# Kernel optimization log

Measured on AMD Instinct MI355X. Metric: run time of the kernel, lower is better.

The kernel has to match this reference:

```python
import jax, jax.numpy as jnp
import numpy as np

B = 64          # batch
NV = 6890       # SMPL vertices
NF = 13776      # SMPL faces
NHD = 20000     # HD (uniformly resampled) vertices
NP = 24         # SMPL parts
COP_W = 10.0
COP_K = 100.0
EPS = 1e-6


def setup_inputs() -> dict:
    key = jax.random.key(0)
    k1, k2, k3, k4, k5 = jax.random.split(key, 5)
    vertices = jax.random.normal(k1, (B, NV, 3), jnp.float32)
    hd_operator = jax.random.uniform(k2, (NHD, NV), jnp.float32) / NV
    faces = jax.random.randint(k3, (NF, 3), 0, NV)          # triangle vertex ids
    vert_fid = jax.random.randint(k4, (NHD,), 0, NF)        # HD vert -> source face
    face_part = jax.random.randint(k5, (NF,), 0, NP)        # face -> body part
    return {"vertices": vertices, "hd_operator": hd_operator,
            "faces": faces, "vert_fid": vert_fid, "face_part": face_part}


def reference(vertices, hd_operator, faces, vert_fid, face_part):
    # --- per-part volume: signed tetrahedron volume per face, summed per part ---
    tri = vertices[:, faces]                      # [B, NF, 3, 3]
    v0, v1, v2 = tri[:, :, 0], tri[:, :, 1], tri[:, :, 2]
    vol_f = jnp.abs(jnp.einsum('bfi,bfi->bf', v0, jnp.cross(v1, v2))) / 6.0  # [B, NF]
    part_onehot = jax.nn.one_hot(face_part, NP, dtype=vol_f.dtype)           # [NF, NP]
    per_part_volume = jnp.einsum('bf,fp->bp', vol_f, part_onehot)            # [B, NP]

    vertices_hd = jnp.einsum('nm,bmd->bnd', hd_operator, vertices)           # [B, NHD, 3]

    # --- map each HD vertex to the volume of its part ---
    part_of_vert = face_part[vert_fid]                                       # [NHD]
    vol_vert = per_part_volume[:, part_of_vert][..., None]                   # [B, NHD, 1]

    # --- volume-weighted COM ---
    com = jnp.sum(vertices_hd * vol_vert, axis=1) / jnp.sum(vol_vert, axis=1)  # [B, 3]

    # --- pressure-weighted COP ---
    h = vertices_hd[:, :, 1]  # vertex height above ground plane (y)
    pw = jnp.where(h < 0.0, 1.0 - COP_K * h, jnp.exp(-COP_W * h))            # [B, NHD]
    cop = jnp.sum(vertices_hd * pw[..., None], axis=1) / (
        jnp.sum(pw, axis=1, keepdims=True) + EPS)                            # [B, 3]

    # --- stability loss: xz distance between COM and COP ---
    d = com - cop
    return jnp.sqrt(d[:, 0] ** 2 + d[:, 2] ** 2)                             # [B]
```

## Files before the change

kernel.cpp:

```cpp
#include <hip/hip_runtime.h>
#include <cstdint>

#define B_    64
#define NV_   6890
#define NF_   13776
#define NHD_  20000
#define NP_   24
#define NCH   216
#define KSPL  4
#define CPW   54

#define OFF_PPV   0u
#define OFF_RED   6144u
#define ZERO_BYTES 7680u
#define OFF_VC    7680u

typedef __attribute__((ext_vector_type(8))) __bf16 bf16x8;
typedef __attribute__((ext_vector_type(8))) unsigned short u16x8;
typedef __attribute__((ext_vector_type(4))) float f32x4;

__device__ __forceinline__ unsigned short f2bf(float f) {
    unsigned u = __float_as_uint(f);
    u = (u + 0x7fffu + ((u >> 16) & 1u)) >> 16;
    return (unsigned short)u;
}

__global__ __launch_bounds__(256) void k0v_pack(const float* __restrict__ verts,
                                                unsigned short* __restrict__ Vc) {
    int idx = blockIdx.x * 256 + threadIdx.x;
    int j    = idx & 7;
    int lane = (idx >> 3) & 63;
    int ct   = idx >> 9;
    int t    = ct % 12;
    int c    = ct / 12;
    int lm   = lane & 15;
    int kk   = (lane >> 4) * 8 + j;
    int bd   = t * 16 + lm;
    int d    = bd >> 6, b = bd & 63;
    int k    = c * 32 + kk;
    float v  = (k < NV_) ? verts[((size_t)b * NV_ + k) * 3 + d] : 0.f;
    Vc[idx] = f2bf(v);
}

__global__ __launch_bounds__(256) void k1_vol(const float* __restrict__ verts,
                                              const int* __restrict__ faces,
                                              const int* __restrict__ face_part,
                                              float* __restrict__ ppv) {
    __shared__ float bins[NP_];
    int b = blockIdx.y;
    int f = blockIdx.x * 256 + threadIdx.x;
    if (threadIdx.x < NP_) bins[threadIdx.x] = 0.f;
    __syncthreads();
    if (f < NF_) {
        int i0 = faces[3 * f], i1 = faces[3 * f + 1], i2 = faces[3 * f + 2];
        const float* vb = verts + (size_t)b * NV_ * 3;
        float ax = vb[3 * i0], ay = vb[3 * i0 + 1], az = vb[3 * i0 + 2];
        float bx = vb[3 * i1], by = vb[3 * i1 + 1], bz = vb[3 * i1 + 2];
        float cx = vb[3 * i2], cy = vb[3 * i2 + 1], cz = vb[3 * i2 + 2];
        float crx = by * cz - bz * cy;
        float cry = bz * cx - bx * cz;
        float crz = bx * cy - by * cx;
        float vol = fabsf(ax * crx + ay * cry + az * crz) * (1.0f / 6.0f);
        atomicAdd(&bins[face_part[f]], vol);
    }
    __syncthreads();
    if (threadIdx.x < NP_) atomicAdd(&ppv[b * NP_ + threadIdx.x], bins[threadIdx.x]);
}

__global__ __launch_bounds__(256, 3) void kf_fused(const float* __restrict__ Hm,
                                                   const unsigned short* __restrict__ Vc,
                                                   const int* __restrict__ vert_fid,
                                                   const int* __restrict__ face_part,
                                                   const float* __restrict__ ppv,
                                                   float* __restrict__ red) {
    __shared__ float accs[16 * 192];
    __shared__ float reds[B_ * 6];
    const int tid  = threadIdx.x;
    const int lane = tid & 63;
    const int s    = tid >> 6;
    const int lm   = lane & 15;
    const int kg   = lane >> 4;
    const int n0   = blockIdx.x * 16;
    const float* Arow = Hm + (size_t)(n0 + lm) * NV_;

    const int cs = s * CPW, ce = cs + CPW;

    f32x4 acc[12];
#pragma unroll
    for (int t = 0; t < 12; ++t) acc[t] = (f32x4){0.f, 0.f, 0.f, 0.f};

    float2 a0, a1, a2, a3, na0, na1, na2, na3;

    auto issueA = [&](int c, float2& b0, float2& b1, float2& b2, float2& b3) {
        int k0 = c * 32 + kg * 8;
        if (c == NCH - 1) {
            float tf[8];
#pragma unroll
            for (int j = 0; j < 8; ++j) {
                int k = k0 + j;
                tf[j] = (k < NV_) ? Arow[k] : 0.f;
            }
            b0 = make_float2(tf[0], tf[1]); b1 = make_float2(tf[2], tf[3]);
            b2 = make_float2(tf[4], tf[5]); b3 = make_float2(tf[6], tf[7]);
        } else {
            b0 = *reinterpret_cast<const float2*>(Arow + k0);
            b1 = *reinterpret_cast<const float2*>(Arow + k0 + 2);
            b2 = *reinterpret_cast<const float2*>(Arow + k0 + 4);
            b3 = *reinterpret_cast<const float2*>(Arow + k0 + 6);
        }
    };

    issueA(cs, a0, a1, a2, a3);
    for (int c = cs; c < ce; ++c) {
        const u16x8* Bp = reinterpret_cast<const u16x8*>(Vc) + (size_t)c * 12 * 64 + lane;
        u16x8 Bu[12];
#pragma unroll
        for (int t = 0; t < 12; ++t) Bu[t] = Bp[t * 64];
        if (c + 1 < ce) issueA(c + 1, na0, na1, na2, na3);
        u16x8 au;
        au[0] = f2bf(a0.x); au[1] = f2bf(a0.y); au[2] = f2bf(a1.x); au[3] = f2bf(a1.y);
        au[4] = f2bf(a2.x); au[5] = f2bf(a2.y); au[6] = f2bf(a3.x); au[7] = f2bf(a3.y);
        bf16x8 Af = __builtin_bit_cast(bf16x8, au);
#pragma unroll
        for (int t = 0; t < 12; ++t)
            acc[t] = __builtin_amdgcn_mfma_f32_16x16x32_bf16(
                Af, __builtin_bit_cast(bf16x8, Bu[t]), acc[t], 0, 0, 0);
        a0 = na0; a1 = na1; a2 = na2; a3 = na3;
    }

    for (int i = tid; i < 16 * 192; i += 256) accs[i] = 0.f;
    for (int i = tid; i < B_ * 6; i += 256) reds[i] = 0.f;
    __syncthreads();
#pragma unroll
    for (int t = 0; t < 12; ++t)
#pragma unroll
        for (int r = 0; r < 4; ++r)
            atomicAdd(&accs[(kg * 4 + r) * 192 + t * 16 + lm], acc[t][r]);
    __syncthreads();

    {
        int b  = tid & 63;
        int r0 = tid >> 6;
        float scx = 0.f, scz = 0.f, smx = 0.f, smz = 0.f, ssp = 0.f, ssw = 0.f;
#pragma unroll
        for (int q = 0; q < 4; ++q) {
            int row = q * 4 + r0;
            int n = n0 + row;
            float x = accs[row * 192 + b];
            float h = accs[row * 192 + 64 + b];
            float z = accs[row * 192 + 128 + b];
            float pwv = (h < 0.f) ? (1.f - 100.f * h) : expf(-10.f * h);
            int part = face_part[vert_fid[n]];
            float w = ppv[b * NP_ + part];
            scx += pwv * x; scz += pwv * z;
            smx += w * x;   smz += w * z;
            ssp += pwv;     ssw += w;
        }
        atomicAdd(&reds[b * 6 + 0], scx);
        atomicAdd(&reds[b * 6 + 1], scz);
        atomicAdd(&reds[b * 6 + 2], smx);
        atomicAdd(&reds[b * 6 + 3], smz);
        atomicAdd(&reds[b * 6 + 4], ssp);
        atomicAdd(&reds[b * 6 + 5], ssw);
    }
    __syncthreads();
    for (int i = tid; i < B_ * 6; i += 256) atomicAdd(&red[i], reds[i]);
}

__global__ __launch_bounds__(64) void k5_final(const float* __restrict__ red,
                                               float* __restrict__ out) {
    int b = threadIdx.x;
    if (b < B_) {
        float sp   = red[b * 6 + 4] + 1e-6f;
        float sw   = red[b * 6 + 5];
        float copx = red[b * 6 + 0] / sp;
        float copz = red[b * 6 + 1] / sp;
        float comx = red[b * 6 + 2] / sw;
        float comz = red[b * 6 + 3] / sw;
        float dx = comx - copx, dz = comz - copz;
        out[b] = sqrtf(dx * dx + dz * dz);
    }
}

extern "C" void kernel_launch(void* const* d_in, const int* in_sizes, int n_in,
                              void* d_out, int out_size, void* d_ws, size_t ws_size,
                              hipStream_t stream) {
    const float* verts     = (const float*)d_in[0];
    const float* Hm        = (const float*)d_in[1];
    const int*   faces     = (const int*)d_in[2];
    const int*   vert_fid  = (const int*)d_in[3];
    const int*   face_part = (const int*)d_in[4];
    char* ws = (char*)d_ws;
    float*          ppv = (float*)(ws + OFF_PPV);
    float*          red = (float*)(ws + OFF_RED);
    unsigned short* Vc  = (unsigned short*)(ws + OFF_VC);
    float* out = (float*)d_out;

    hipMemsetAsync(d_ws, 0, ZERO_BYTES, stream);
    hipLaunchKernelGGL(k0v_pack, dim3((NCH * 12 * 512) / 256), dim3(256), 0, stream, verts, Vc);
    hipLaunchKernelGGL(k1_vol, dim3(54, 64), dim3(256), 0, stream, verts, faces, face_part, ppv);
    hipLaunchKernelGGL(kf_fused, dim3(NHD_ / 16), dim3(256), 0, stream,
                       Hm, Vc, vert_fid, face_part, ppv, red);
    hipLaunchKernelGGL(k5_final, dim3(1), dim3(64), 0, stream, red, out);
}
```

Before: 312.6 us.

## Process 32 HD rows per block to reuse packed vertex tiles across two MFMA sets

```diff
diff --git a/kernel.cpp b/kernel.cpp
--- a/kernel.cpp
+++ b/kernel.cpp
@@ -67,101 +67,116 @@
     if (threadIdx.x < NP_) atomicAdd(&ppv[b * NP_ + threadIdx.x], bins[threadIdx.x]);
 }
 
-__global__ __launch_bounds__(256, 3) void kf_fused(const float* __restrict__ Hm,
-                                                   const unsigned short* __restrict__ Vc,
-                                                   const int* __restrict__ vert_fid,
-                                                   const int* __restrict__ face_part,
-                                                   const float* __restrict__ ppv,
-                                                   float* __restrict__ red) {
-    __shared__ float accs[16 * 192];
+#define ACCP 193
+__global__ __launch_bounds__(256) void kf_fused(const float* __restrict__ Hm,
+                                                const unsigned short* __restrict__ Vc,
+                                                const int* __restrict__ vert_fid,
+                                                const int* __restrict__ face_part,
+                                                const float* __restrict__ ppv,
+                                                float* __restrict__ red) {
+    __shared__ float accs[32 * ACCP];
     __shared__ float reds[B_ * 6];
     const int tid  = threadIdx.x;
     const int lane = tid & 63;
     const int s    = tid >> 6;
     const int lm   = lane & 15;
     const int kg   = lane >> 4;
-    const int n0   = blockIdx.x * 16;
-    const float* Arow = Hm + (size_t)(n0 + lm) * NV_;
-
+    const int n0   = blockIdx.x * 32;
+    const float* Arow0 = Hm + (size_t)(n0 + lm) * NV_;
+    const float* Arow1 = Hm + (size_t)(n0 + 16 + lm) * NV_;
     const int cs = s * CPW, ce = cs + CPW;
 
-    f32x4 acc[12];
-#pragma unroll
-    for (int t = 0; t < 12; ++t) acc[t] = (f32x4){0.f, 0.f, 0.f, 0.f};
-
-    float2 a0, a1, a2, a3, na0, na1, na2, na3;
-
-    auto issueA = [&](int c, float2& b0, float2& b1, float2& b2, float2& b3) {
+    f32x4 acc0[12], acc1[12];
+#pragma unroll
+    for (int t = 0; t < 12; ++t) {
+        acc0[t] = (f32x4){0.f, 0.f, 0.f, 0.f};
+        acc1[t] = (f32x4){0.f, 0.f, 0.f, 0.f};
+    }
+
+    float2 a[4], b[4], na[4], nb[4];
+
+    auto issueA = [&](int c, const float* R, float2* dst) {
         int k0 = c * 32 + kg * 8;
         if (c == NCH - 1) {
             float tf[8];
 #pragma unroll
             for (int j = 0; j < 8; ++j) {
                 int k = k0 + j;
-                tf[j] = (k < NV_) ? Arow[k] : 0.f;
+                tf[j] = (k < NV_) ? R[k] : 0.f;
             }
-            b0 = make_float2(tf[0], tf[1]); b1 = make_float2(tf[2], tf[3]);
-            b2 = make_float2(tf[4], tf[5]); b3 = make_float2(tf[6], tf[7]);
+            dst[0] = make_float2(tf[0], tf[1]); dst[1] = make_float2(tf[2], tf[3]);
+            dst[2] = make_float2(tf[4], tf[5]); dst[3] = make_float2(tf[6], tf[7]);
         } else {
-            b0 = *reinterpret_cast<const float2*>(Arow + k0);
-            b1 = *reinterpret_cast<const float2*>(Arow + k0 + 2);
-            b2 = *reinterpret_cast<const float2*>(Arow + k0 + 4);
-            b3 = *reinterpret_cast<const float2*>(Arow + k0 + 6);
+            dst[0] = *reinterpret_cast<const float2*>(R + k0);
+            dst[1] = *reinterpret_cast<const float2*>(R + k0 + 2);
+            dst[2] = *reinterpret_cast<const float2*>(R + k0 + 4);
+            dst[3] = *reinterpret_cast<const float2*>(R + k0 + 6);
         }
     };
 
-    issueA(cs, a0, a1, a2, a3);
+    issueA(cs, Arow0, a);
+    issueA(cs, Arow1, b);
     for (int c = cs; c < ce; ++c) {
         const u16x8* Bp = reinterpret_cast<const u16x8*>(Vc) + (size_t)c * 12 * 64 + lane;
         u16x8 Bu[12];
 #pragma unroll
         for (int t = 0; t < 12; ++t) Bu[t] = Bp[t * 64];
-        if (c + 1 < ce) issueA(c + 1, na0, na1, na2, na3);
-        u16x8 au;
-        au[0] = f2bf(a0.x); au[1] = f2bf(a0.y); au[2] = f2bf(a1.x); au[3] = f2bf(a1.y);
-        au[4] = f2bf(a2.x); au[5] = f2bf(a2.y); au[6] = f2bf(a3.x); au[7] = f2bf(a3.y);
-        bf16x8 Af = __builtin_bit_cast(bf16x8, au);
+        if (c + 1 < ce) { issueA(c + 1, Arow0, na); issueA(c + 1, Arow1, nb); }
+        u16x8 au0, au1;
+        au0[0] = f2bf(a[0].x); au0[1] = f2bf(a[0].y); au0[2] = f2bf(a[1].x); au0[3] = f2bf(a[1].y);
+        au0[4] = f2bf(a[2].x); au0[5] = f2bf(a[2].y); au0[6] = f2bf(a[3].x); au0[7] = f2bf(a[3].y);
+        au1[0] = f2bf(b[0].x); au1[1] = f2bf(b[0].y); au1[2] = f2bf(b[1].x); au1[3] = f2bf(b[1].y);
+        au1[4] = f2bf(b[2].x); au1[5] = f2bf(b[2].y); au1[6] = f2bf(b[3].x); au1[7] = f2bf(b[3].y);
+        bf16x8 Af0 = __builtin_bit_cast(bf16x8, au0);
+        bf16x8 Af1 = __builtin_bit_cast(bf16x8, au1);
 #pragma unroll
         for (int t = 0; t < 12; ++t)
-            acc[t] = __builtin_amdgcn_mfma_f32_16x16x32_bf16(
-                Af, __builtin_bit_cast(bf16x8, Bu[t]), acc[t], 0, 0, 0);
-        a0 = na0; a1 = na1; a2 = na2; a3 = na3;
-    }
-
-    for (int i = tid; i < 16 * 192; i += 256) accs[i] = 0.f;
+            acc0[t] = __builtin_amdgcn_mfma_f32_16x16x32_bf16(
+                Af0, __builtin_bit_cast(bf16x8, Bu[t]), acc0[t], 0, 0, 0);
+#pragma unroll
+        for (int t = 0; t < 12; ++t)
+            acc1[t] = __builtin_amdgcn_mfma_f32_16x16x32_bf16(
+                Af1, __builtin_bit_cast(bf16x8, Bu[t]), acc1[t], 0, 0, 0);
+#pragma unroll
+        for (int j = 0; j < 4; ++j) { a[j] = na[j]; b[j] = nb[j]; }
+    }
+
+    for (int i = tid; i < 32 * ACCP; i += 256) accs[i] = 0.f;
     for (int i = tid; i < B_ * 6; i += 256) reds[i] = 0.f;
     __syncthreads();
 #pragma unroll
     for (int t = 0; t < 12; ++t)
 #pragma unroll
-        for (int r = 0; r < 4; ++r)
-            atomicAdd(&accs[(kg * 4 + r) * 192 + t * 16 + lm], acc[t][r]);
+        for (int r = 0; r < 4; ++r) {
+            atomicAdd(&accs[(kg * 4 + r) * ACCP + t * 16 + lm], acc0[t][r]);
+            atomicAdd(&accs[(16 + kg * 4 + r) * ACCP + t * 16 + lm], acc1[t][r]);
+        }
     __syncthreads();
 
     {
-        int b  = tid & 63;
+        int bb = tid & 63;
         int r0 = tid >> 6;
         float scx = 0.f, scz = 0.f, smx = 0.f, smz = 0.f, ssp = 0.f, ssw = 0.f;
 #pragma unroll
-        for (int q = 0; q < 4; ++q) {
+        for (int q = 0; q < 8; ++q) {
             int row = q * 4 + r0;
             int n = n0 + row;
-            float x = accs[row * 192 + b];
-            float h = accs[row * 192 + 64 + b];
-            float z = accs[row * 192 + 128 + b];
+            float x = accs[row * ACCP + bb];
+            float h = accs[row * ACCP + 64 + bb];
+            float z = accs[row * ACCP + 128 + bb];
             float pwv = (h < 0.f) ? (1.f - 100.f * h) : expf(-10.f * h);
             int part = face_part[vert_fid[n]];
-            float w = ppv[b * NP_ + part];
+            float w = ppv[bb * NP_ + part];
             scx += pwv * x; scz += pwv * z;
             smx += w * x;   smz += w * z;
             ssp += pwv;     ssw += w;
         }
-        atomicAdd(&reds[b * 6 + 0], scx);
-        atomicAdd(&reds[b * 6 + 1], scz);
-        atomicAdd(&reds[b * 6 + 2], smx);
-        atomicAdd(&reds[b * 6 + 3], smz);
-        atomicAdd(&reds[b * 6 + 4], ssp);
-        atomicAdd(&reds[b * 6 + 5], ssw);
+        atomicAdd(&reds[bb * 6 + 0], scx);
+        atomicAdd(&reds[bb * 6 + 1], scz);
+        atomicAdd(&reds[bb * 6 + 2], smx);
+        atomicAdd(&reds[bb * 6 + 3], smz);
+        atomicAdd(&reds[bb * 6 + 4], ssp);
+        atomicAdd(&reds[bb * 6 + 5], ssw);
     }
     __syncthreads();
     for (int i = tid; i < B_ * 6; i += 256) atomicAdd(&red[i], reds[i]);
@@ -199,7 +214,7 @@
     hipMemsetAsync(d_ws, 0, ZERO_BYTES, stream);
     hipLaunchKernelGGL(k0v_pack, dim3((NCH * 12 * 512) / 256), dim3(256), 0, stream, verts, Vc);
     hipLaunchKernelGGL(k1_vol, dim3(54, 64), dim3(256), 0, stream, verts, faces, face_part, ppv);
-    hipLaunchKernelGGL(kf_fused, dim3(NHD_ / 16), dim3(256), 0, stream,
+    hipLaunchKernelGGL(kf_fused, dim3(NHD_ / 32), dim3(256), 0, stream,
                        Hm, Vc, vert_fid, face_part, ppv, red);
     hipLaunchKernelGGL(k5_final, dim3(1), dim3(64), 0, stream, red, out);
 }
```

Result: faster. 303.5 us (-2.9%).
